# Kernel tuning notes

Measured on AMD Instinct MI355X. Metric: run time of the kernel, lower is better.

## Reference

```python
import jax, jax.numpy as jnp
import numpy as np

M, K, N = 8192, 4096, 12288


def setup_inputs() -> dict:
    key = jax.random.key(0)
    k1, k2, k3, k4 = jax.random.split(key, 4)
    input_tensor = jax.random.normal(k1, (1, M, K), dtype=jnp.float32)
    # int8 quantized weight [N, K] and per-output-channel scale [N, 1]
    weight = jax.random.randint(k2, (N, K), -127, 128, dtype=jnp.int32).astype(jnp.int8)
    weight_scale = (jax.random.uniform(k3, (N, 1), dtype=jnp.float32) * 0.01 + 1e-4)
    bias = jax.random.normal(k4, (N,), dtype=jnp.float32) * 0.1
    return {"input_tensor": input_tensor, "weight": weight,
            "weight_scale": weight_scale, "bias": bias}


def reference(input_tensor, weight, weight_scale, bias):
    x = input_tensor[0]  # squeeze(0) -> [M, K]
    # dynamic per-token symmetric int8 quantization: scale = absmax/127
    a_scale = jnp.max(jnp.abs(x), axis=-1, keepdims=True) / 127.0  # [M, 1]
    q = jnp.clip(jnp.round(x / a_scale), -128.0, 127.0)  # int8 values held in f32
    # int8 GEMM accumulated (emulated in f32), then dequant with per-token x per-channel scales
    acc = jnp.einsum('mk,nk->mn', q, weight.astype(jnp.float32))  # [M, N]
    out = acc * a_scale * weight_scale[:, 0][None, :] + bias[None, :]
    return out[None].astype(input_tensor.dtype)  # unsqueeze(0) -> [1, M, N]
```

## Files before the change

kernel.cpp:

```cpp
#include <hip/hip_runtime.h>
#include <cstdint>

#define M_DIM 8192
#define K_DIM 4096
#define N_DIM 12288
#define KT 32

using i32x4 = __attribute__((ext_vector_type(4))) int;

__device__ inline void gload_lds16(const void* g, void* l) {
    __builtin_amdgcn_global_load_lds(
        (const __attribute__((address_space(1))) void*)g,
        (__attribute__((address_space(3))) void*)l,
        16, 0, 0);
}

__global__ __launch_bounds__(256) void quant_pack(const float* __restrict__ x,
                                                  const int* __restrict__ w32,
                                                  int8_t* __restrict__ qa,
                                                  float* __restrict__ ascale,
                                                  int8_t* __restrict__ wq) {
    const int t = threadIdx.x;
    if (blockIdx.x < M_DIM) {
        const int row = blockIdx.x;
        const float4* xr = (const float4*)(x + (size_t)row * K_DIM);
        float4 v[4];
        float amax = 0.0f;
#pragma unroll
        for (int c = 0; c < 4; ++c) {
            v[c] = xr[t + 256 * c];
            amax = fmaxf(amax, fmaxf(fmaxf(fabsf(v[c].x), fabsf(v[c].y)),
                                     fmaxf(fabsf(v[c].z), fabsf(v[c].w))));
        }
#pragma unroll
        for (int off = 32; off > 0; off >>= 1)
            amax = fmaxf(amax, __shfl_xor(amax, off));
        __shared__ float smax[4];
        if ((t & 63) == 0) smax[t >> 6] = amax;
        __syncthreads();
        amax = fmaxf(fmaxf(smax[0], smax[1]), fmaxf(smax[2], smax[3]));
        const float sc = amax * (1.0f / 127.0f);
        const float inv = (amax > 0.0f) ? (127.0f / amax) : 0.0f;
        if (t == 0) ascale[row] = sc;

        int* q32 = (int*)(qa + (size_t)row * K_DIM);
#pragma unroll
        for (int c = 0; c < 4; ++c) {
            int q0 = (int)rintf(v[c].x * inv);
            int q1 = (int)rintf(v[c].y * inv);
            int q2 = (int)rintf(v[c].z * inv);
            int q3 = (int)rintf(v[c].w * inv);
            q0 = min(127, max(-128, q0));
            q1 = min(127, max(-128, q1));
            q2 = min(127, max(-128, q2));
            q3 = min(127, max(-128, q3));
            q32[t + 256 * c] = (q0 & 255) | ((q1 & 255) << 8) | ((q2 & 255) << 16) | (q3 << 24);
        }
    } else {
        const int pb = blockIdx.x - M_DIM;
        const size_t total4 = (size_t)N_DIM * K_DIM / 4;
        const size_t stride = (size_t)2048 * 256;
        int* out32 = (int*)wq;
        for (size_t i = (size_t)pb * 256 + t; i < total4; i += stride) {
            const int4 v = ((const int4*)w32)[i];
            out32[i] = (v.x & 255) | ((v.y & 255) << 8) | ((v.z & 255) << 16) | (v.w << 24);
        }
    }
}

__global__ __launch_bounds__(512, 2) void gemm_i8(const int8_t* __restrict__ qa,
                                                  const int8_t* __restrict__ wq,
                                                  const float* __restrict__ ascale,
                                                  const float* __restrict__ wscale,
                                                  const float* __restrict__ bias,
                                                  float* __restrict__ out) {
    __shared__ int8_t lds[2][2][32768];

    const int t = threadIdx.x;
    const int lane = t & 63;
    const int wave = t >> 6;
    const int wm = wave >> 2;
    const int wn = wave & 3;
    const int lrow = lane & 15;
    const int lk = lane >> 4;
    const int sw7 = lrow & 7;

    const int flat = blockIdx.x;
    const int sw = (flat & 7) * 192 + (flat >> 3);
    const int bm = sw / 48;
    const int bn = sw % 48;

    const int srow = t >> 3;
    const int g = (t & 7) ^ (srow & 7);

#define STAGE_OP(ptr, sb, op, rowbase, jt)                                     \
    {                                                                          \
        _Pragma("unroll") for (int c = 0; c < 4; ++c)                          \
            gload_lds16(ptr + (size_t)((rowbase) + srow + 64 * c) * K_DIM +    \
                            (size_t)g * 16 + (size_t)(jt) * 128,               \
                        &lds[sb][op][c * 8192 + t * 16]);                      \
    }

#define READ_A(dst, LA, mh)                                                    \
    {                                                                          \
        _Pragma("unroll") for (int mf = 0; mf < 4; ++mf)                       \
            _Pragma("unroll") for (int ks = 0; ks < 2; ++ks)                   \
                dst[mf][ks] = *(const i32x4*)&LA[(wm * 128 + (mh)*64 +         \
                                                 mf * 16 + lrow) * 128 +       \
                                                ((((ks << 2) | lk) ^ sw7) << 4)]; \
    }
#define READ_B(dst, LB, nh)                                                    \
    {                                                                          \
        _Pragma("unroll") for (int nf = 0; nf < 2; ++nf)                       \
            _Pragma("unroll") for (int ks = 0; ks < 2; ++ks)                   \
                dst[nf][ks] = *(const i32x4*)&LB[(wn * 64 + (nh)*32 +          \
                                                 nf * 16 + lrow) * 128 +       \
                                                ((((ks << 2) | lk) ^ sw7) << 4)]; \
    }
#define MM(AH, BH, mh, nh)                                                     \
    {                                                                          \
        __builtin_amdgcn_s_setprio(1);                                         \
        _Pragma("unroll") for (int ks = 0; ks < 2; ++ks)                       \
            _Pragma("unroll") for (int mf = 0; mf < 4; ++mf)                   \
                _Pragma("unroll") for (int nf = 0; nf < 2; ++nf)               \
                    acc[(mh)*4 + mf][(nh)*2 + nf] =                            \
                        __builtin_amdgcn_mfma_i32_16x16x64_i8(                 \
                            AH[mf][ks], BH[nf][ks],                            \
                            acc[(mh)*4 + mf][(nh)*2 + nf], 0, 0, 0);           \
        __builtin_amdgcn_s_setprio(0);                                         \
    }
#define LGKM0_PIN                                                              \
    asm volatile("s_waitcnt lgkmcnt(0)" ::: "memory");                         \
    __builtin_amdgcn_sched_barrier(0);

    i32x4 acc[8][4] = {};
    i32x4 a0[4][2], a1[4][2], b0[2][2], b1[2][2];

    STAGE_OP(qa, 0, 0, bm * 256, 0);
    STAGE_OP(wq, 0, 1, bn * 256, 0);

    for (int j = 0; j < KT; ++j) {
        const int cs = j & 1;
        const int ns = cs ^ 1;
        const int8_t* __restrict__ LA = lds[cs][0];
        const int8_t* __restrict__ LB = lds[cs][1];

        if (j + 1 < KT) {
            STAGE_OP(qa, ns, 0, bm * 256, j + 1);
            asm volatile("s_waitcnt vmcnt(4)" ::: "memory");
        } else {
            asm volatile("s_waitcnt vmcnt(0)" ::: "memory");
        }
        __builtin_amdgcn_s_barrier();
        __builtin_amdgcn_sched_barrier(0);
        READ_A(a0, LA, 0);
        READ_B(b0, LB, 0);
        LGKM0_PIN;
        MM(a0, b0, 0, 0);

        READ_B(b1, LB, 1);
        if (j + 1 < KT) STAGE_OP(wq, ns, 1, bn * 256, j + 1);
        __builtin_amdgcn_s_barrier();
        LGKM0_PIN;
        MM(a0, b1, 0, 1);

        READ_A(a1, LA, 1);
        __builtin_amdgcn_s_barrier();
        LGKM0_PIN;
        MM(a1, b1, 1, 1);

        __builtin_amdgcn_s_barrier();
        __builtin_amdgcn_sched_barrier(0);
        MM(a1, b0, 1, 0);
    }

    const int r0 = bm * 256 + wm * 128;
    const int c0 = bn * 256 + wn * 64;
    float asc[8][4];
#pragma unroll
    for (int m = 0; m < 8; ++m)
#pragma unroll
        for (int jj = 0; jj < 4; ++jj)
            asc[m][jj] = ascale[r0 + m * 16 + lk * 4 + jj];
#pragma unroll
    for (int n = 0; n < 4; ++n) {
        const int col = c0 + n * 16 + lrow;
        const float wsc = wscale[col];
        const float bb = bias[col];
#pragma unroll
        for (int m = 0; m < 8; ++m) {
#pragma unroll
            for (int jj = 0; jj < 4; ++jj) {
                const int row = r0 + m * 16 + lk * 4 + jj;
                out[(size_t)row * N_DIM + col] = (float)acc[m][n][jj] * asc[m][jj] * wsc + bb;
            }
        }
    }
}

extern "C" void kernel_launch(void* const* d_in, const int* in_sizes, int n_in,
                              void* d_out, int out_size, void* d_ws, size_t ws_size,
                              hipStream_t stream) {
    const float* x = (const float*)d_in[0];
    const int* w32 = (const int*)d_in[1];
    const float* wscale = (const float*)d_in[2];
    const float* bias = (const float*)d_in[3];
    float* out = (float*)d_out;

    int8_t* qa = (int8_t*)d_ws;
    float* ascale = (float*)((char*)d_ws + (size_t)M_DIM * K_DIM);
    int8_t* wq = (int8_t*)((char*)d_ws + (size_t)M_DIM * K_DIM +
                           (size_t)M_DIM * sizeof(float));

    quant_pack<<<M_DIM + 2048, 256, 0, stream>>>(x, w32, qa, ascale, wq);
    gemm_i8<<<1536, 512, 0, stream>>>(qa, wq, ascale, wscale, bias, out);
}
```

Baseline: 503.5 us.

## Pre-pack weights into MFMA fragment order and load B directly to registers

The weight packing pass now writes int8 weights in a per-wave, per-k-tile fragment layout that matches the MFMA B operand. The GEMM loads B fragments straight from global memory into registers, double-buffered across iterations, and only A is staged through LDS. This halves LDS use and removes the B LDS reads and several barriers per k-step. In exchange, each wave fetches its B fragments from global memory on its own (the two M-waves sharing a column no longer share an LDS copy), which adds global/L2 traffic and register pressure, and the pack kernel uses a strided gather.

```diff
diff --git a/kernel.cpp b/kernel.cpp
--- a/kernel.cpp
+++ b/kernel.cpp
@@ -15,11 +15,15 @@
         16, 0, 0);
 }
 
+__device__ inline int pack4(int4 v) {
+    return (v.x & 255) | ((v.y & 255) << 8) | ((v.z & 255) << 16) | (v.w << 24);
+}
+
 __global__ __launch_bounds__(256) void quant_pack(const float* __restrict__ x,
                                                   const int* __restrict__ w32,
                                                   int8_t* __restrict__ qa,
                                                   float* __restrict__ ascale,
-                                                  int8_t* __restrict__ wq) {
+                                                  int8_t* __restrict__ wb) {
     const int t = threadIdx.x;
     if (blockIdx.x < M_DIM) {
         const int row = blockIdx.x;
@@ -58,23 +62,36 @@
         }
     } else {
         const int pb = blockIdx.x - M_DIM;
-        const size_t total4 = (size_t)N_DIM * K_DIM / 4;
+        const size_t total = (size_t)N_DIM * K_DIM / 16;
         const size_t stride = (size_t)2048 * 256;
-        int* out32 = (int*)wq;
-        for (size_t i = (size_t)pb * 256 + t; i < total4; i += stride) {
-            const int4 v = ((const int4*)w32)[i];
-            out32[i] = (v.x & 255) | ((v.y & 255) << 8) | ((v.z & 255) << 16) | (v.w << 24);
+        for (size_t i = (size_t)pb * 256 + t; i < total; i += stride) {
+            const uint32_t c = (uint32_t)i;
+            const int lr = c & 15;
+            const int lk = (c >> 4) & 3;
+            const uint32_t q = c >> 6;
+            const int ks = q & 1;
+            const int nf = (q >> 1) & 3;
+            const uint32_t r = q >> 3;
+            const int j = r & 31;
+            const uint32_t s2 = r >> 5;
+            const int n = (int)(s2 >> 2) * 256 + (int)(s2 & 3) * 64 + nf * 16 + lr;
+            const int k0 = j * 128 + (ks * 4 + lk) * 16;
+            const int4* src = (const int4*)(w32 + (size_t)n * K_DIM + k0);
+            const int4 v0 = src[0], v1 = src[1], v2 = src[2], v3 = src[3];
+            i32x4 o;
+            o[0] = pack4(v0); o[1] = pack4(v1); o[2] = pack4(v2); o[3] = pack4(v3);
+            ((i32x4*)wb)[i] = o;
         }
     }
 }
 
 __global__ __launch_bounds__(512, 2) void gemm_i8(const int8_t* __restrict__ qa,
-                                                  const int8_t* __restrict__ wq,
+                                                  const int8_t* __restrict__ wb,
                                                   const float* __restrict__ ascale,
                                                   const float* __restrict__ wscale,
                                                   const float* __restrict__ bias,
                                                   float* __restrict__ out) {
-    __shared__ int8_t lds[2][2][32768];
+    __shared__ int8_t lds[2][32768];
 
     const int t = threadIdx.x;
     const int lane = t & 63;
@@ -93,85 +110,91 @@
     const int srow = t >> 3;
     const int g = (t & 7) ^ (srow & 7);
 
-#define STAGE_OP(ptr, sb, op, rowbase, jt)                                     \
+#define STAGE_A(sb, jt)                                                        \
     {                                                                          \
         _Pragma("unroll") for (int c = 0; c < 4; ++c)                          \
-            gload_lds16(ptr + (size_t)((rowbase) + srow + 64 * c) * K_DIM +    \
+            gload_lds16(qa + (size_t)(bm * 256 + srow + 64 * c) * K_DIM +      \
                             (size_t)g * 16 + (size_t)(jt) * 128,               \
-                        &lds[sb][op][c * 8192 + t * 16]);                      \
-    }
-
-#define READ_A(dst, LA, mh)                                                    \
+                        &lds[sb][c * 8192 + t * 16]);                          \
+    }
+#define READ_A(dst, cs, mh)                                                    \
     {                                                                          \
         _Pragma("unroll") for (int mf = 0; mf < 4; ++mf)                       \
             _Pragma("unroll") for (int ks = 0; ks < 2; ++ks)                   \
-                dst[mf][ks] = *(const i32x4*)&LA[(wm * 128 + (mh)*64 +         \
-                                                 mf * 16 + lrow) * 128 +       \
-                                                ((((ks << 2) | lk) ^ sw7) << 4)]; \
-    }
-#define READ_B(dst, LB, nh)                                                    \
+                dst[mf][ks] = *(const i32x4*)&lds[cs][(wm * 128 + (mh)*64 +    \
+                                                      mf * 16 + lrow) * 128 + \
+                                                     ((((ks << 2) | lk) ^ sw7) << 4)]; \
+    }
+    const int8_t* wbase = wb + (size_t)(bn * 4 + wn) * 262144 + (size_t)lane * 16;
+#define LOAD_BLO(jt)                                                           \
     {                                                                          \
         _Pragma("unroll") for (int nf = 0; nf < 2; ++nf)                       \
             _Pragma("unroll") for (int ks = 0; ks < 2; ++ks)                   \
-                dst[nf][ks] = *(const i32x4*)&LB[(wn * 64 + (nh)*32 +          \
-                                                 nf * 16 + lrow) * 128 +       \
-                                                ((((ks << 2) | lk) ^ sw7) << 4)]; \
-    }
-#define MM(AH, BH, mh, nh)                                                     \
+                bLo[nf][ks] = *(const i32x4*)(wbase + (size_t)(jt)*8192 +      \
+                                              (nf * 2 + ks) * 1024);           \
+    }
+#define LOAD_BHI(jt)                                                           \
+    {                                                                          \
+        _Pragma("unroll") for (int nf = 0; nf < 2; ++nf)                       \
+            _Pragma("unroll") for (int ks = 0; ks < 2; ++ks)                   \
+                bHi[nf][ks] = *(const i32x4*)(wbase + (size_t)(jt)*8192 +      \
+                                              ((nf + 2) * 2 + ks) * 1024);     \
+    }
+#define MM8(AH, mb, BH, nb)                                                    \
     {                                                                          \
         __builtin_amdgcn_s_setprio(1);                                         \
         _Pragma("unroll") for (int ks = 0; ks < 2; ++ks)                       \
             _Pragma("unroll") for (int mf = 0; mf < 4; ++mf)                   \
                 _Pragma("unroll") for (int nf = 0; nf < 2; ++nf)               \
-                    acc[(mh)*4 + mf][(nh)*2 + nf] =                            \
+                    acc[(mb) + mf][(nb) + nf] =                                \
                         __builtin_amdgcn_mfma_i32_16x16x64_i8(                 \
                             AH[mf][ks], BH[nf][ks],                            \
-                            acc[(mh)*4 + mf][(nh)*2 + nf], 0, 0, 0);           \
+                            acc[(mb) + mf][(nb) + nf], 0, 0, 0);               \
         __builtin_amdgcn_s_setprio(0);                                         \
     }
-#define LGKM0_PIN                                                              \
-    asm volatile("s_waitcnt lgkmcnt(0)" ::: "memory");                         \
-    __builtin_amdgcn_sched_barrier(0);
+#define SB0 __builtin_amdgcn_sched_barrier(0);
+#define BAR __builtin_amdgcn_s_barrier();
+#define WAIT_LGKM(n) asm volatile("s_waitcnt lgkmcnt(" #n ")" ::: "memory");
+#define WAIT_VM(n) asm volatile("s_waitcnt vmcnt(" #n ")" ::: "memory");
 
     i32x4 acc[8][4] = {};
-    i32x4 a0[4][2], a1[4][2], b0[2][2], b1[2][2];
-
-    STAGE_OP(qa, 0, 0, bm * 256, 0);
-    STAGE_OP(wq, 0, 1, bn * 256, 0);
+    i32x4 a0[4][2], a1[4][2], bLo[2][2], bHi[2][2];
+
+    STAGE_A(0, 0);
+    LOAD_BLO(0);
+    LOAD_BHI(0);
+    SB0;
 
     for (int j = 0; j < KT; ++j) {
         const int cs = j & 1;
         const int ns = cs ^ 1;
-        const int8_t* __restrict__ LA = lds[cs][0];
-        const int8_t* __restrict__ LB = lds[cs][1];
-
+
+        WAIT_VM(4);
+        SB0;
+        BAR;
+        SB0;
+        if (j + 1 < KT) STAGE_A(ns, j + 1);
+        READ_A(a0, cs, 0);
+        READ_A(a1, cs, 1);
+        SB0;
+        WAIT_LGKM(8);
+        SB0;
+        MM8(a0, 0, bLo, 0);
+        WAIT_LGKM(0);
+        SB0;
+        MM8(a1, 4, bLo, 0);
         if (j + 1 < KT) {
-            STAGE_OP(qa, ns, 0, bm * 256, j + 1);
-            asm volatile("s_waitcnt vmcnt(4)" ::: "memory");
+            LOAD_BLO(j + 1);
+            SB0;
+            WAIT_VM(8);
         } else {
-            asm volatile("s_waitcnt vmcnt(0)" ::: "memory");
-        }
-        __builtin_amdgcn_s_barrier();
-        __builtin_amdgcn_sched_barrier(0);
-        READ_A(a0, LA, 0);
-        READ_B(b0, LB, 0);
-        LGKM0_PIN;
-        MM(a0, b0, 0, 0);
-
-        READ_B(b1, LB, 1);
-        if (j + 1 < KT) STAGE_OP(wq, ns, 1, bn * 256, j + 1);
-        __builtin_amdgcn_s_barrier();
-        LGKM0_PIN;
-        MM(a0, b1, 0, 1);
-
-        READ_A(a1, LA, 1);
-        __builtin_amdgcn_s_barrier();
-        LGKM0_PIN;
-        MM(a1, b1, 1, 1);
-
-        __builtin_amdgcn_s_barrier();
-        __builtin_amdgcn_sched_barrier(0);
-        MM(a1, b0, 1, 0);
+            WAIT_VM(0);
+        }
+        SB0;
+        MM8(a1, 4, bHi, 2);
+        MM8(a0, 0, bHi, 2);
+        if (j + 1 < KT) LOAD_BHI(j + 1);
+        SB0;
     }
 
     const int r0 = bm * 256 + wm * 128;
@@ -209,9 +232,9 @@
 
     int8_t* qa = (int8_t*)d_ws;
     float* ascale = (float*)((char*)d_ws + (size_t)M_DIM * K_DIM);
-    int8_t* wq = (int8_t*)((char*)d_ws + (size_t)M_DIM * K_DIM +
+    int8_t* wb = (int8_t*)((char*)d_ws + (size_t)M_DIM * K_DIM +
                            (size_t)M_DIM * sizeof(float));
 
-    quant_pack<<<M_DIM + 2048, 256, 0, stream>>>(x, w32, qa, ascale, wq);
-    gemm_i8<<<1536, 512, 0, stream>>>(qa, wq, ascale, wscale, bias, out);
-}
+    quant_pack<<<M_DIM + 2048, 256, 0, stream>>>(x, w32, qa, ascale, wb);
+    gemm_i8<<<1536, 512, 0, stream>>>(qa, wb, ascale, wscale, bias, out);
+}
```

Measured after the change: 552.9 us. 1.1x slower.
